# Performance work log

Measured on AMD Instinct MI355X. Metric: run time of the kernel, lower is better.

Reference implementation:

```python
import jax, jax.numpy as jnp
import numpy as np

B, T, C = 4, 2048, 1024
H = 16
D = C // H  # 64


def setup_inputs() -> dict:
    key = jax.random.key(0)
    ks = jax.random.split(key, 3)
    scale = 1.0 / np.sqrt(C)
    return {
        "x": jax.random.normal(ks[0], (B, T, C), dtype=jnp.float32),
        "W_attn": jax.random.normal(ks[1], (C, 3 * C), dtype=jnp.float32) * scale,
        "b_attn": jnp.zeros((3 * C,), dtype=jnp.float32),
        "W_proj": jax.random.normal(ks[2], (C, C), dtype=jnp.float32) * scale,
        "b_proj": jnp.zeros((C,), dtype=jnp.float32),
    }


def reference(x, W_attn, b_attn, W_proj, b_proj):
    b, t, c = x.shape
    qkv = x @ W_attn + b_attn                      # [B,T,3C]
    q, k, v = jnp.split(qkv, 3, axis=-1)           # each [B,T,C]
    to_heads = lambda z: z.reshape(b, t, H, D).transpose(0, 2, 1, 3)  # [B,H,T,D]
    q, k, v = to_heads(q), to_heads(k), to_heads(v)
    scores = jnp.einsum("bhtd,bhsd->bhts", q, k) / jnp.sqrt(jnp.float32(D))
    causal = jnp.tril(jnp.ones((t, t), dtype=bool))  # [T,T]
    scores = jnp.where(causal[None, None], scores, jnp.finfo(scores.dtype).min)
    attn = jax.nn.softmax(scores, axis=-1)           # [B,H,T,T]
    out = jnp.einsum("bhts,bhsd->bhtd", attn, v)     # [B,H,T,D]
    out = out.transpose(0, 2, 1, 3).reshape(b, t, c)
    return out @ W_proj + b_proj
```

## Files before the change

### kernel.cpp

```cpp
#include <hip/hip_runtime.h>
#include <hip/hip_bf16.h>

typedef __bf16 bf16_t;
typedef __attribute__((ext_vector_type(8))) __bf16 bf16x8;
typedef __attribute__((ext_vector_type(4))) float f32x4;
typedef __attribute__((ext_vector_type(4))) unsigned short u16x4;

#define B_DIM 4
#define T_DIM 2048
#define C_DIM 1024
#define H_DIM 16
#define D_DIM 64
#define M_TOK (B_DIM * T_DIM)
#define N_QKV (3 * C_DIM)
#define NT    (T_DIM / 64)
#define KSTR  72
#define CSC   0.18033688011112042f

__device__ __forceinline__ void gload_lds16(const bf16_t* g, bf16_t* l) {
  __builtin_amdgcn_global_load_lds((const __attribute__((address_space(1))) void*)(g),
                                   (__attribute__((address_space(3))) void*)(l), 16, 0, 0);
}

__global__ void cvt_f32_to_bf16(const float* __restrict__ in, bf16_t* __restrict__ out, int n4) {
  int i = blockIdx.x * blockDim.x + threadIdx.x;
  if (i >= n4) return;
  float4 v = ((const float4*)in)[i];
  struct alignas(8) bv4 { bf16_t x, y, z, w; };
  bv4 o;
  o.x = (bf16_t)v.x; o.y = (bf16_t)v.y; o.z = (bf16_t)v.z; o.w = (bf16_t)v.w;
  ((bv4*)out)[i] = o;
}

__global__ void transpose_f32_to_bf16(const float* __restrict__ in, bf16_t* __restrict__ out,
                                      int K, int N) {
  __shared__ float tile[32][33];
  int bx = blockIdx.x * 32;
  int by = blockIdx.y * 32;
  int tx = threadIdx.x, ty = threadIdx.y;
#pragma unroll
  for (int i = 0; i < 32; i += 8)
    tile[ty + i][tx] = in[(size_t)(by + ty + i) * N + bx + tx];
  __syncthreads();
#pragma unroll
  for (int i = 0; i < 32; i += 8)
    out[(size_t)(bx + ty + i) * K + by + tx] = (bf16_t)tile[tx][ty + i];
}

#define BM 128
#define BN 128
#define BK 32

__global__ __launch_bounds__(256, 4)
void gemm_bt_bias(const bf16_t* __restrict__ A, const bf16_t* __restrict__ Bt,
                  const float* __restrict__ bias, bf16_t* __restrict__ Cb,
                  int M, int N, int K) {
  __shared__ alignas(16) bf16_t As[BM * BK];
  __shared__ alignas(16) bf16_t Bs[BN * BK];
  const int tid = threadIdx.x;
  const int lane = tid & 63;
  const int wave = tid >> 6;
  const int wr = (wave >> 1) * 64, wc = (wave & 1) * 64;
  const int quad = lane >> 4, l16 = lane & 15;
  const int row0 = blockIdx.x * BM, col0 = blockIdx.y * BN;

  const int srow = wave * 32 + (lane >> 2);
  const int scol = (lane & 3) * 8;
  const bf16_t* Ag = A + (size_t)(row0 + srow) * K + scol;
  const bf16_t* Bg = Bt + (size_t)(col0 + srow) * K + scol;
  bf16_t* AsW = &As[(wave * 32) * BK];
  bf16_t* BsW = &Bs[(wave * 32) * BK];

  f32x4 acc[4][4];
#pragma unroll
  for (int i = 0; i < 4; ++i)
#pragma unroll
    for (int j = 0; j < 4; ++j)
      acc[i][j] = (f32x4){0.f, 0.f, 0.f, 0.f};

  for (int k0 = 0; k0 < K; k0 += BK) {
    __syncthreads();
    gload_lds16(Ag + k0, AsW);
    gload_lds16(Ag + k0 + (size_t)16 * K, AsW + 16 * BK);
    gload_lds16(Bg + k0, BsW);
    gload_lds16(Bg + k0 + (size_t)16 * K, BsW + 16 * BK);
    __syncthreads();
    bf16x8 af[4], bfr[4];
#pragma unroll
    for (int i = 0; i < 4; ++i)
      af[i] = *(const bf16x8*)&As[(wr + i * 16 + l16) * BK + quad * 8];
#pragma unroll
    for (int j = 0; j < 4; ++j)
      bfr[j] = *(const bf16x8*)&Bs[(wc + j * 16 + l16) * BK + quad * 8];
#pragma unroll
    for (int i = 0; i < 4; ++i)
#pragma unroll
      for (int j = 0; j < 4; ++j)
        acc[i][j] = __builtin_amdgcn_mfma_f32_16x16x32_bf16(af[i], bfr[j], acc[i][j], 0, 0, 0);
  }

#pragma unroll
  for (int i = 0; i < 4; ++i)
#pragma unroll
    for (int j = 0; j < 4; ++j) {
      int col = col0 + wc + j * 16 + l16;
      float bv = bias[col];
#pragma unroll
      for (int r = 0; r < 4; ++r) {
        int row = row0 + wr + i * 16 + quad * 4 + r;
        Cb[(size_t)row * N + col] = (bf16_t)(acc[i][j][r] + bv);
      }
    }
}

__global__ __launch_bounds__(256, 4)
void gemm_bt_bias_n64(const bf16_t* __restrict__ A, const bf16_t* __restrict__ Bt,
                      const float* __restrict__ bias, float* __restrict__ Cf,
                      int M, int N, int K) {
  __shared__ alignas(16) bf16_t As[BM * BK];
  __shared__ alignas(16) bf16_t Bs[64 * BK];
  const int tid = threadIdx.x;
  const int lane = tid & 63;
  const int wave = tid >> 6;
  const int wr = (wave >> 1) * 64, wc = (wave & 1) * 32;
  const int quad = lane >> 4, l16 = lane & 15;
  const int row0 = blockIdx.x * BM, col0 = blockIdx.y * 64;

  const int sr = lane >> 2;
  const int scol = (lane & 3) * 8;
  const bf16_t* Ag = A + (size_t)(row0 + wave * 32 + sr) * K + scol;
  const bf16_t* Bg = Bt + (size_t)(col0 + wave * 16 + sr) * K + scol;
  bf16_t* AsW = &As[(wave * 32) * BK];
  bf16_t* BsW = &Bs[(wave * 16) * BK];

  f32x4 acc[4][2];
#pragma unroll
  for (int i = 0; i < 4; ++i)
#pragma unroll
    for (int j = 0; j < 2; ++j)
      acc[i][j] = (f32x4){0.f, 0.f, 0.f, 0.f};

  for (int k0 = 0; k0 < K; k0 += BK) {
    __syncthreads();
    gload_lds16(Ag + k0, AsW);
    gload_lds16(Ag + k0 + (size_t)16 * K, AsW + 16 * BK);
    gload_lds16(Bg + k0, BsW);
    __syncthreads();
    bf16x8 af[4], bfr[2];
#pragma unroll
    for (int i = 0; i < 4; ++i)
      af[i] = *(const bf16x8*)&As[(wr + i * 16 + l16) * BK + quad * 8];
#pragma unroll
    for (int j = 0; j < 2; ++j)
      bfr[j] = *(const bf16x8*)&Bs[(wc + j * 16 + l16) * BK + quad * 8];
#pragma unroll
    for (int i = 0; i < 4; ++i)
#pragma unroll
      for (int j = 0; j < 2; ++j)
        acc[i][j] = __builtin_amdgcn_mfma_f32_16x16x32_bf16(af[i], bfr[j], acc[i][j], 0, 0, 0);
  }

#pragma unroll
  for (int i = 0; i < 4; ++i)
#pragma unroll
    for (int j = 0; j < 2; ++j) {
      int col = col0 + wc + j * 16 + l16;
      float bv = bias[col];
#pragma unroll
      for (int r = 0; r < 4; ++r) {
        int row = row0 + wr + i * 16 + quad * 4 + r;
        Cf[(size_t)row * N + col] = acc[i][j][r] + bv;
      }
    }
}

__device__ __forceinline__ float exp_row_sum(f32x4 sv[4], bool diag, bf16_t* PsW,
                                             int l16, int quad, int wave) {
  if (diag) {
    const int qr = wave * 16 + l16;
#pragma unroll
    for (int ct = 0; ct < 4; ++ct)
#pragma unroll
      for (int r = 0; r < 4; ++r)
        if (ct * 16 + quad * 4 + r > qr) sv[ct][r] = -INFINITY;
  }
  float rsum = 0.f;
#pragma unroll
  for (int ct = 0; ct < 4; ++ct) {
    u16x4 pk;
#pragma unroll
    for (int r = 0; r < 4; ++r) {
      float p = __builtin_amdgcn_exp2f(sv[ct][r] * CSC);
      rsum += p;
      pk[r] = __builtin_bit_cast(unsigned short, (bf16_t)p);
    }
    *(u16x4*)&PsW[l16 * KSTR + ct * 16 + quad * 4] = pk;
  }
  rsum += __shfl_xor(rsum, 16);
  rsum += __shfl_xor(rsum, 32);
  return rsum;
}

__global__ __launch_bounds__(256, 4)
void attn_fwd(const bf16_t* __restrict__ qkv, bf16_t* __restrict__ out) {
  __shared__ alignas(16) bf16_t Ks[64 * KSTR];
  __shared__ alignas(16) bf16_t Vt[64 * KSTR];
  __shared__ alignas(16) bf16_t Ps[4 * 16 * KSTR];

  const int tid = threadIdx.x;
  const int lane = tid & 63;
  const int wave = tid >> 6;
  const int quad = lane >> 4, l16 = lane & 15;
  const int qlo = blockIdx.x;
  const int qhi = NT - 1 - qlo;
  const int h = blockIdx.y, b = blockIdx.z;
  const size_t tokBase = (size_t)b * T_DIM;

  const bf16_t* qpl = qkv + (tokBase + qlo * 64 + wave * 16 + l16) * N_QKV + h * D_DIM;
  const bf16_t* qph = qkv + (tokBase + qhi * 64 + wave * 16 + l16) * N_QKV + h * D_DIM;
  bf16x8 ql0 = *(const bf16x8*)(qpl + quad * 8);
  bf16x8 ql1 = *(const bf16x8*)(qpl + 32 + quad * 8);
  bf16x8 qh0 = *(const bf16x8*)(qph + quad * 8);
  bf16x8 qh1 = *(const bf16x8*)(qph + 32 + quad * 8);

  f32x4 ol[4], oh[4];
#pragma unroll
  for (int dt = 0; dt < 4; ++dt) {
    ol[dt] = (f32x4){0.f, 0.f, 0.f, 0.f};
    oh[dt] = (f32x4){0.f, 0.f, 0.f, 0.f};
  }
  float ll = 0.f, lh = 0.f;

  const int tx = tid & 15, ty = tid >> 4;
  const int vswz = ((tx >> 2) & 3) * 8;
  bf16_t* PsW = &Ps[wave * 16 * KSTR];
  const f32x4 zero4 = (f32x4){0.f, 0.f, 0.f, 0.f};

  u16x4 kreg[4], vreg[4];
  const bf16_t* kb0 = qkv + (tokBase + ty * 4) * N_QKV + h * D_DIM + C_DIM + tx * 4;
#pragma unroll
  for (int r = 0; r < 4; ++r) kreg[r] = *(const u16x4*)(kb0 + (size_t)r * N_QKV);
#pragma unroll
  for (int r = 0; r < 4; ++r) vreg[r] = *(const u16x4*)(kb0 + (size_t)r * N_QKV + C_DIM);

  for (int t = 0; t <= qhi; ++t) {
    const bool lo = (t <= qlo);
    __syncthreads();
#pragma unroll
    for (int r = 0; r < 4; ++r)
      *(u16x4*)&Ks[(ty * 4 + r) * KSTR + tx * 4] = kreg[r];
#pragma unroll
    for (int i = 0; i < 4; ++i) {
      u16x4 p = (u16x4){vreg[0][i], vreg[1][i], vreg[2][i], vreg[3][i]};
      *(u16x4*)&Vt[(tx * 4 + i) * KSTR + ((ty * 4) ^ vswz)] = p;
    }
    __syncthreads();
    if (t < qhi) {
      const bf16_t* kb = qkv + (tokBase + (t + 1) * 64 + ty * 4) * N_QKV + h * D_DIM + C_DIM + tx * 4;
#pragma unroll
      for (int r = 0; r < 4; ++r) kreg[r] = *(const u16x4*)(kb + (size_t)r * N_QKV);
#pragma unroll
      for (int r = 0; r < 4; ++r) vreg[r] = *(const u16x4*)(kb + (size_t)r * N_QKV + C_DIM);
    }

    f32x4 svl[4], svh[4];
#pragma unroll
    for (int ct = 0; ct < 4; ++ct) {
      bf16x8 kf0 = *(const bf16x8*)&Ks[(ct * 16 + l16) * KSTR + quad * 8];
      bf16x8 kf1 = *(const bf16x8*)&Ks[(ct * 16 + l16) * KSTR + 32 + quad * 8];
      if (lo) {
        svl[ct] = __builtin_amdgcn_mfma_f32_16x16x32_bf16(kf0, ql0, zero4, 0, 0, 0);
        svl[ct] = __builtin_amdgcn_mfma_f32_16x16x32_bf16(kf1, ql1, svl[ct], 0, 0, 0);
      }
      svh[ct] = __builtin_amdgcn_mfma_f32_16x16x32_bf16(kf0, qh0, zero4, 0, 0, 0);
      svh[ct] = __builtin_amdgcn_mfma_f32_16x16x32_bf16(kf1, qh1, svh[ct], 0, 0, 0);
    }

    bf16x8 pl0, pl1, ph0, ph1;
    if (lo) {
      ll += exp_row_sum(svl, t == qlo, PsW, l16, quad, wave);
      pl0 = *(const bf16x8*)&PsW[l16 * KSTR + quad * 8];
      pl1 = *(const bf16x8*)&PsW[l16 * KSTR + 32 + quad * 8];
    }
    lh += exp_row_sum(svh, t == qhi, PsW, l16, quad, wave);
    ph0 = *(const bf16x8*)&PsW[l16 * KSTR + quad * 8];
    ph1 = *(const bf16x8*)&PsW[l16 * KSTR + 32 + quad * 8];

#pragma unroll
    for (int dt = 0; dt < 4; ++dt) {
      const int vcol = (quad * 8) ^ ((dt & 3) * 8);
      bf16x8 vf0 = *(const bf16x8*)&Vt[(dt * 16 + l16) * KSTR + vcol];
      bf16x8 vf1 = *(const bf16x8*)&Vt[(dt * 16 + l16) * KSTR + 32 + vcol];
      if (lo) {
        ol[dt] = __builtin_amdgcn_mfma_f32_16x16x32_bf16(vf0, pl0, ol[dt], 0, 0, 0);
        ol[dt] = __builtin_amdgcn_mfma_f32_16x16x32_bf16(vf1, pl1, ol[dt], 0, 0, 0);
      }
      oh[dt] = __builtin_amdgcn_mfma_f32_16x16x32_bf16(vf0, ph0, oh[dt], 0, 0, 0);
      oh[dt] = __builtin_amdgcn_mfma_f32_16x16x32_bf16(vf1, ph1, oh[dt], 0, 0, 0);
    }
  }

  struct alignas(8) bh4 { bf16_t a, b, c, d; };
  {
    float rl = 1.0f / ll;
    bf16_t* op = out + (tokBase + qlo * 64 + wave * 16 + l16) * C_DIM + h * D_DIM;
#pragma unroll
    for (int dt = 0; dt < 4; ++dt) {
      bh4 v = {(bf16_t)(ol[dt][0] * rl), (bf16_t)(ol[dt][1] * rl),
               (bf16_t)(ol[dt][2] * rl), (bf16_t)(ol[dt][3] * rl)};
      *(bh4*)(op + dt * 16 + quad * 4) = v;
    }
  }
  {
    float rl = 1.0f / lh;
    bf16_t* op = out + (tokBase + qhi * 64 + wave * 16 + l16) * C_DIM + h * D_DIM;
#pragma unroll
    for (int dt = 0; dt < 4; ++dt) {
      bh4 v = {(bf16_t)(oh[dt][0] * rl), (bf16_t)(oh[dt][1] * rl),
               (bf16_t)(oh[dt][2] * rl), (bf16_t)(oh[dt][3] * rl)};
      *(bh4*)(op + dt * 16 + quad * 4) = v;
    }
  }
}

extern "C" void kernel_launch(void* const* d_in, const int* in_sizes, int n_in,
                              void* d_out, int out_size, void* d_ws, size_t ws_size,
                              hipStream_t stream) {
  const float* x      = (const float*)d_in[0];
  const float* W_attn = (const float*)d_in[1];
  const float* b_attn = (const float*)d_in[2];
  const float* W_proj = (const float*)d_in[3];
  const float* b_proj = (const float*)d_in[4];
  float* out = (float*)d_out;

  char* ws = (char*)d_ws;
  bf16_t* xb   = (bf16_t*)ws;  ws += (size_t)M_TOK * C_DIM * 2;
  bf16_t* Wat  = (bf16_t*)ws;  ws += (size_t)N_QKV * C_DIM * 2;
  bf16_t* Wpt  = (bf16_t*)ws;  ws += (size_t)C_DIM * C_DIM * 2;
  bf16_t* qkv  = (bf16_t*)ws;  ws += (size_t)M_TOK * N_QKV * 2;
  bf16_t* attn = (bf16_t*)ws;  ws += (size_t)M_TOK * C_DIM * 2;

  {
    int n4 = (M_TOK * C_DIM) / 4;
    cvt_f32_to_bf16<<<n4 / 256, 256, 0, stream>>>(x, xb, n4);
  }
  transpose_f32_to_bf16<<<dim3(N_QKV / 32, C_DIM / 32), dim3(32, 8), 0, stream>>>(W_attn, Wat, C_DIM, N_QKV);
  transpose_f32_to_bf16<<<dim3(C_DIM / 32, C_DIM / 32), dim3(32, 8), 0, stream>>>(W_proj, Wpt, C_DIM, C_DIM);

  gemm_bt_bias<<<dim3(M_TOK / BM, N_QKV / BN), 256, 0, stream>>>(
      xb, Wat, b_attn, qkv, M_TOK, N_QKV, C_DIM);

  attn_fwd<<<dim3(NT / 2, H_DIM, B_DIM), 256, 0, stream>>>(qkv, attn);

  gemm_bt_bias_n64<<<dim3(M_TOK / BM, C_DIM / 64), 256, 0, stream>>>(
      attn, Wpt, b_proj, out, M_TOK, C_DIM, C_DIM);
}
```

Baseline: 266.2 us.

## Keep softmax probabilities in registers and use one query tile per block

The attention kernel no longer pairs a low and high query tile per block. Each block now handles a single tile, with a rotated blockIdx-to-tile mapping to spread causal work across the grid. The P tile no longer round-trips through LDS: the V transpose store uses a permuted column layout so the exponentiated scores can be packed directly into the MFMA B operand. This removes the Ps buffer and its LDS traffic, and the launch bound is raised to 8 blocks, but per-block work becomes uneven and K/V tiles are reloaded once per query tile.

```diff
diff --git a/kernel.cpp b/kernel.cpp
--- a/kernel.cpp
+++ b/kernel.cpp
@@ -5,6 +5,7 @@
 typedef __attribute__((ext_vector_type(8))) __bf16 bf16x8;
 typedef __attribute__((ext_vector_type(4))) float f32x4;
 typedef __attribute__((ext_vector_type(4))) unsigned short u16x4;
+typedef __attribute__((ext_vector_type(4))) unsigned int u32x4;
 
 #define B_DIM 4
 #define T_DIM 2048
@@ -174,66 +175,31 @@
     }
 }
 
-__device__ __forceinline__ float exp_row_sum(f32x4 sv[4], bool diag, bf16_t* PsW,
-                                             int l16, int quad, int wave) {
-  if (diag) {
-    const int qr = wave * 16 + l16;
-#pragma unroll
-    for (int ct = 0; ct < 4; ++ct)
-#pragma unroll
-      for (int r = 0; r < 4; ++r)
-        if (ct * 16 + quad * 4 + r > qr) sv[ct][r] = -INFINITY;
-  }
-  float rsum = 0.f;
-#pragma unroll
-  for (int ct = 0; ct < 4; ++ct) {
-    u16x4 pk;
-#pragma unroll
-    for (int r = 0; r < 4; ++r) {
-      float p = __builtin_amdgcn_exp2f(sv[ct][r] * CSC);
-      rsum += p;
-      pk[r] = __builtin_bit_cast(unsigned short, (bf16_t)p);
-    }
-    *(u16x4*)&PsW[l16 * KSTR + ct * 16 + quad * 4] = pk;
-  }
-  rsum += __shfl_xor(rsum, 16);
-  rsum += __shfl_xor(rsum, 32);
-  return rsum;
-}
-
-__global__ __launch_bounds__(256, 4)
+__global__ __launch_bounds__(256, 8)
 void attn_fwd(const bf16_t* __restrict__ qkv, bf16_t* __restrict__ out) {
   __shared__ alignas(16) bf16_t Ks[64 * KSTR];
   __shared__ alignas(16) bf16_t Vt[64 * KSTR];
-  __shared__ alignas(16) bf16_t Ps[4 * 16 * KSTR];
 
   const int tid = threadIdx.x;
   const int lane = tid & 63;
   const int wave = tid >> 6;
   const int quad = lane >> 4, l16 = lane & 15;
-  const int qlo = blockIdx.x;
-  const int qhi = NT - 1 - qlo;
   const int h = blockIdx.y, b = blockIdx.z;
+  const int q = (int)((blockIdx.x + h + 2 * b) & 31);
   const size_t tokBase = (size_t)b * T_DIM;
 
-  const bf16_t* qpl = qkv + (tokBase + qlo * 64 + wave * 16 + l16) * N_QKV + h * D_DIM;
-  const bf16_t* qph = qkv + (tokBase + qhi * 64 + wave * 16 + l16) * N_QKV + h * D_DIM;
-  bf16x8 ql0 = *(const bf16x8*)(qpl + quad * 8);
-  bf16x8 ql1 = *(const bf16x8*)(qpl + 32 + quad * 8);
-  bf16x8 qh0 = *(const bf16x8*)(qph + quad * 8);
-  bf16x8 qh1 = *(const bf16x8*)(qph + 32 + quad * 8);
-
-  f32x4 ol[4], oh[4];
-#pragma unroll
-  for (int dt = 0; dt < 4; ++dt) {
-    ol[dt] = (f32x4){0.f, 0.f, 0.f, 0.f};
-    oh[dt] = (f32x4){0.f, 0.f, 0.f, 0.f};
-  }
-  float ll = 0.f, lh = 0.f;
+  const bf16_t* qp = qkv + (tokBase + q * 64 + wave * 16 + l16) * N_QKV + h * D_DIM;
+  bf16x8 q0 = *(const bf16x8*)(qp + quad * 8);
+  bf16x8 q1 = *(const bf16x8*)(qp + 32 + quad * 8);
+
+  f32x4 o[4];
+#pragma unroll
+  for (int dt = 0; dt < 4; ++dt) o[dt] = (f32x4){0.f, 0.f, 0.f, 0.f};
+  float lsum = 0.f;
 
   const int tx = tid & 15, ty = tid >> 4;
   const int vswz = ((tx >> 2) & 3) * 8;
-  bf16_t* PsW = &Ps[wave * 16 * KSTR];
+  const int vcol = (8 * (ty & 3) + 4 * ((ty >> 2) & 1) + 32 * (ty >> 3)) ^ vswz;
   const f32x4 zero4 = (f32x4){0.f, 0.f, 0.f, 0.f};
 
   u16x4 kreg[4], vreg[4];
@@ -243,8 +209,7 @@
 #pragma unroll
   for (int r = 0; r < 4; ++r) vreg[r] = *(const u16x4*)(kb0 + (size_t)r * N_QKV + C_DIM);
 
-  for (int t = 0; t <= qhi; ++t) {
-    const bool lo = (t <= qlo);
+  for (int t = 0; t <= q; ++t) {
     __syncthreads();
 #pragma unroll
     for (int r = 0; r < 4; ++r)
@@ -252,10 +217,10 @@
 #pragma unroll
     for (int i = 0; i < 4; ++i) {
       u16x4 p = (u16x4){vreg[0][i], vreg[1][i], vreg[2][i], vreg[3][i]};
-      *(u16x4*)&Vt[(tx * 4 + i) * KSTR + ((ty * 4) ^ vswz)] = p;
-    }
-    __syncthreads();
-    if (t < qhi) {
+      *(u16x4*)&Vt[(tx * 4 + i) * KSTR + vcol] = p;
+    }
+    __syncthreads();
+    if (t < q) {
       const bf16_t* kb = qkv + (tokBase + (t + 1) * 64 + ty * 4) * N_QKV + h * D_DIM + C_DIM + tx * 4;
 #pragma unroll
       for (int r = 0; r < 4; ++r) kreg[r] = *(const u16x4*)(kb + (size_t)r * N_QKV);
@@ -263,61 +228,65 @@
       for (int r = 0; r < 4; ++r) vreg[r] = *(const u16x4*)(kb + (size_t)r * N_QKV + C_DIM);
     }
 
-    f32x4 svl[4], svh[4];
+    f32x4 sv[4];
 #pragma unroll
     for (int ct = 0; ct < 4; ++ct) {
       bf16x8 kf0 = *(const bf16x8*)&Ks[(ct * 16 + l16) * KSTR + quad * 8];
       bf16x8 kf1 = *(const bf16x8*)&Ks[(ct * 16 + l16) * KSTR + 32 + quad * 8];
-      if (lo) {
-        svl[ct] = __builtin_amdgcn_mfma_f32_16x16x32_bf16(kf0, ql0, zero4, 0, 0, 0);
-        svl[ct] = __builtin_amdgcn_mfma_f32_16x16x32_bf16(kf1, ql1, svl[ct], 0, 0, 0);
-      }
-      svh[ct] = __builtin_amdgcn_mfma_f32_16x16x32_bf16(kf0, qh0, zero4, 0, 0, 0);
-      svh[ct] = __builtin_amdgcn_mfma_f32_16x16x32_bf16(kf1, qh1, svh[ct], 0, 0, 0);
-    }
-
-    bf16x8 pl0, pl1, ph0, ph1;
-    if (lo) {
-      ll += exp_row_sum(svl, t == qlo, PsW, l16, quad, wave);
-      pl0 = *(const bf16x8*)&PsW[l16 * KSTR + quad * 8];
-      pl1 = *(const bf16x8*)&PsW[l16 * KSTR + 32 + quad * 8];
-    }
-    lh += exp_row_sum(svh, t == qhi, PsW, l16, quad, wave);
-    ph0 = *(const bf16x8*)&PsW[l16 * KSTR + quad * 8];
-    ph1 = *(const bf16x8*)&PsW[l16 * KSTR + 32 + quad * 8];
+      sv[ct] = __builtin_amdgcn_mfma_f32_16x16x32_bf16(kf0, q0, zero4, 0, 0, 0);
+      sv[ct] = __builtin_amdgcn_mfma_f32_16x16x32_bf16(kf1, q1, sv[ct], 0, 0, 0);
+    }
+    if (t == q) {
+      const int qr = wave * 16 + l16;
+#pragma unroll
+      for (int ct = 0; ct < 4; ++ct)
+#pragma unroll
+        for (int r = 0; r < 4; ++r)
+          if (ct * 16 + quad * 4 + r > qr) sv[ct][r] = -INFINITY;
+    }
+
+    float rsum = 0.f;
+    unsigned int lw[8];
+    struct alignas(4) bpair { bf16_t lo, hi; };
+#pragma unroll
+    for (int ct = 0; ct < 4; ++ct) {
+      float e0 = __builtin_amdgcn_exp2f(sv[ct][0] * CSC);
+      float e1 = __builtin_amdgcn_exp2f(sv[ct][1] * CSC);
+      float e2 = __builtin_amdgcn_exp2f(sv[ct][2] * CSC);
+      float e3 = __builtin_amdgcn_exp2f(sv[ct][3] * CSC);
+      rsum += (e0 + e1) + (e2 + e3);
+      bpair w0 = {(bf16_t)e0, (bf16_t)e1};
+      bpair w1 = {(bf16_t)e2, (bf16_t)e3};
+      lw[ct * 2 + 0] = __builtin_bit_cast(unsigned int, w0);
+      lw[ct * 2 + 1] = __builtin_bit_cast(unsigned int, w1);
+    }
+    rsum += __shfl_xor(rsum, 16);
+    rsum += __shfl_xor(rsum, 32);
+    lsum += rsum;
+
+    u32x4 pw0 = (u32x4){lw[0], lw[1], lw[2], lw[3]};
+    u32x4 pw1 = (u32x4){lw[4], lw[5], lw[6], lw[7]};
+    bf16x8 p0 = __builtin_bit_cast(bf16x8, pw0);
+    bf16x8 p1 = __builtin_bit_cast(bf16x8, pw1);
 
 #pragma unroll
     for (int dt = 0; dt < 4; ++dt) {
-      const int vcol = (quad * 8) ^ ((dt & 3) * 8);
-      bf16x8 vf0 = *(const bf16x8*)&Vt[(dt * 16 + l16) * KSTR + vcol];
-      bf16x8 vf1 = *(const bf16x8*)&Vt[(dt * 16 + l16) * KSTR + 32 + vcol];
-      if (lo) {
-        ol[dt] = __builtin_amdgcn_mfma_f32_16x16x32_bf16(vf0, pl0, ol[dt], 0, 0, 0);
-        ol[dt] = __builtin_amdgcn_mfma_f32_16x16x32_bf16(vf1, pl1, ol[dt], 0, 0, 0);
-      }
-      oh[dt] = __builtin_amdgcn_mfma_f32_16x16x32_bf16(vf0, ph0, oh[dt], 0, 0, 0);
-      oh[dt] = __builtin_amdgcn_mfma_f32_16x16x32_bf16(vf1, ph1, oh[dt], 0, 0, 0);
+      const int vc = (quad * 8) ^ (dt * 8);
+      bf16x8 vf0 = *(const bf16x8*)&Vt[(dt * 16 + l16) * KSTR + vc];
+      bf16x8 vf1 = *(const bf16x8*)&Vt[(dt * 16 + l16) * KSTR + 32 + vc];
+      o[dt] = __builtin_amdgcn_mfma_f32_16x16x32_bf16(vf0, p0, o[dt], 0, 0, 0);
+      o[dt] = __builtin_amdgcn_mfma_f32_16x16x32_bf16(vf1, p1, o[dt], 0, 0, 0);
     }
   }
 
   struct alignas(8) bh4 { bf16_t a, b, c, d; };
   {
-    float rl = 1.0f / ll;
-    bf16_t* op = out + (tokBase + qlo * 64 + wave * 16 + l16) * C_DIM + h * D_DIM;
+    float rl = 1.0f / lsum;
+    bf16_t* op = out + (tokBase + q * 64 + wave * 16 + l16) * C_DIM + h * D_DIM;
 #pragma unroll
     for (int dt = 0; dt < 4; ++dt) {
-      bh4 v = {(bf16_t)(ol[dt][0] * rl), (bf16_t)(ol[dt][1] * rl),
-               (bf16_t)(ol[dt][2] * rl), (bf16_t)(ol[dt][3] * rl)};
-      *(bh4*)(op + dt * 16 + quad * 4) = v;
-    }
-  }
-  {
-    float rl = 1.0f / lh;
-    bf16_t* op = out + (tokBase + qhi * 64 + wave * 16 + l16) * C_DIM + h * D_DIM;
-#pragma unroll
-    for (int dt = 0; dt < 4; ++dt) {
-      bh4 v = {(bf16_t)(oh[dt][0] * rl), (bf16_t)(oh[dt][1] * rl),
-               (bf16_t)(oh[dt][2] * rl), (bf16_t)(oh[dt][3] * rl)};
+      bh4 v = {(bf16_t)(o[dt][0] * rl), (bf16_t)(o[dt][1] * rl),
+               (bf16_t)(o[dt][2] * rl), (bf16_t)(o[dt][3] * rl)};
       *(bh4*)(op + dt * 16 + quad * 4) = v;
     }
   }
@@ -350,7 +319,7 @@
   gemm_bt_bias<<<dim3(M_TOK / BM, N_QKV / BN), 256, 0, stream>>>(
       xb, Wat, b_attn, qkv, M_TOK, N_QKV, C_DIM);
 
-  attn_fwd<<<dim3(NT / 2, H_DIM, B_DIM), 256, 0, stream>>>(qkv, attn);
+  attn_fwd<<<dim3(NT, H_DIM, B_DIM), 256, 0, stream>>>(qkv, attn);
 
   gemm_bt_bias_n64<<<dim3(M_TOK / BM, C_DIM / 64), 256, 0, stream>>>(
       attn, Wpt, b_proj, out, M_TOK, C_DIM, C_DIM);
```

Measured after the change: 317.9 us. 1.19x slower.

## Keep softmax probabilities in registers by permuting V's key layout in LDS

Applied to the files above, without the earlier changes.

Drops the per-wave LDS staging buffer for P. The exponentiated scores are now packed straight into the MFMA B-operand registers, and the V tile is stored in LDS with its key dimension permuted so it matches the register layout of P from the S MFMA output. This removes an LDS write/read round trip and the LDS footprint of P on every key tile. The cost is a more intricate index mapping for V, and correctness depends on that permutation matching exactly.

```diff
diff --git a/kernel.cpp b/kernel.cpp
--- a/kernel.cpp
+++ b/kernel.cpp
@@ -5,6 +5,7 @@
 typedef __attribute__((ext_vector_type(8))) __bf16 bf16x8;
 typedef __attribute__((ext_vector_type(4))) float f32x4;
 typedef __attribute__((ext_vector_type(4))) unsigned short u16x4;
+typedef __attribute__((ext_vector_type(4))) unsigned int u32x4;
 
 #define B_DIM 4
 #define T_DIM 2048
@@ -174,38 +175,10 @@
     }
 }
 
-__device__ __forceinline__ float exp_row_sum(f32x4 sv[4], bool diag, bf16_t* PsW,
-                                             int l16, int quad, int wave) {
-  if (diag) {
-    const int qr = wave * 16 + l16;
-#pragma unroll
-    for (int ct = 0; ct < 4; ++ct)
-#pragma unroll
-      for (int r = 0; r < 4; ++r)
-        if (ct * 16 + quad * 4 + r > qr) sv[ct][r] = -INFINITY;
-  }
-  float rsum = 0.f;
-#pragma unroll
-  for (int ct = 0; ct < 4; ++ct) {
-    u16x4 pk;
-#pragma unroll
-    for (int r = 0; r < 4; ++r) {
-      float p = __builtin_amdgcn_exp2f(sv[ct][r] * CSC);
-      rsum += p;
-      pk[r] = __builtin_bit_cast(unsigned short, (bf16_t)p);
-    }
-    *(u16x4*)&PsW[l16 * KSTR + ct * 16 + quad * 4] = pk;
-  }
-  rsum += __shfl_xor(rsum, 16);
-  rsum += __shfl_xor(rsum, 32);
-  return rsum;
-}
-
 __global__ __launch_bounds__(256, 4)
 void attn_fwd(const bf16_t* __restrict__ qkv, bf16_t* __restrict__ out) {
   __shared__ alignas(16) bf16_t Ks[64 * KSTR];
   __shared__ alignas(16) bf16_t Vt[64 * KSTR];
-  __shared__ alignas(16) bf16_t Ps[4 * 16 * KSTR];
 
   const int tid = threadIdx.x;
   const int lane = tid & 63;
@@ -233,7 +206,7 @@
 
   const int tx = tid & 15, ty = tid >> 4;
   const int vswz = ((tx >> 2) & 3) * 8;
-  bf16_t* PsW = &Ps[wave * 16 * KSTR];
+  const int vcol = (8 * (ty & 3) + 4 * ((ty >> 2) & 1) + 32 * (ty >> 3)) ^ vswz;
   const f32x4 zero4 = (f32x4){0.f, 0.f, 0.f, 0.f};
 
   u16x4 kreg[4], vreg[4];
@@ -252,7 +225,7 @@
 #pragma unroll
     for (int i = 0; i < 4; ++i) {
       u16x4 p = (u16x4){vreg[0][i], vreg[1][i], vreg[2][i], vreg[3][i]};
-      *(u16x4*)&Vt[(tx * 4 + i) * KSTR + ((ty * 4) ^ vswz)] = p;
+      *(u16x4*)&Vt[(tx * 4 + i) * KSTR + vcol] = p;
     }
     __syncthreads();
     if (t < qhi) {
@@ -275,22 +248,77 @@
       svh[ct] = __builtin_amdgcn_mfma_f32_16x16x32_bf16(kf0, qh0, zero4, 0, 0, 0);
       svh[ct] = __builtin_amdgcn_mfma_f32_16x16x32_bf16(kf1, qh1, svh[ct], 0, 0, 0);
     }
-
+    if (t == qlo) {
+      const int qr = wave * 16 + l16;
+#pragma unroll
+      for (int ct = 0; ct < 4; ++ct)
+#pragma unroll
+        for (int r = 0; r < 4; ++r)
+          if (ct * 16 + quad * 4 + r > qr) svl[ct][r] = -INFINITY;
+    }
+    if (t == qhi) {
+      const int qr = wave * 16 + l16;
+#pragma unroll
+      for (int ct = 0; ct < 4; ++ct)
+#pragma unroll
+        for (int r = 0; r < 4; ++r)
+          if (ct * 16 + quad * 4 + r > qr) svh[ct][r] = -INFINITY;
+    }
+
+    struct alignas(4) bpair { bf16_t lo, hi; };
     bf16x8 pl0, pl1, ph0, ph1;
     if (lo) {
-      ll += exp_row_sum(svl, t == qlo, PsW, l16, quad, wave);
-      pl0 = *(const bf16x8*)&PsW[l16 * KSTR + quad * 8];
-      pl1 = *(const bf16x8*)&PsW[l16 * KSTR + 32 + quad * 8];
-    }
-    lh += exp_row_sum(svh, t == qhi, PsW, l16, quad, wave);
-    ph0 = *(const bf16x8*)&PsW[l16 * KSTR + quad * 8];
-    ph1 = *(const bf16x8*)&PsW[l16 * KSTR + 32 + quad * 8];
+      float rsum = 0.f;
+      unsigned int lw[8];
+#pragma unroll
+      for (int ct = 0; ct < 4; ++ct) {
+        float e0 = __builtin_amdgcn_exp2f(svl[ct][0] * CSC);
+        float e1 = __builtin_amdgcn_exp2f(svl[ct][1] * CSC);
+        float e2 = __builtin_amdgcn_exp2f(svl[ct][2] * CSC);
+        float e3 = __builtin_amdgcn_exp2f(svl[ct][3] * CSC);
+        rsum += (e0 + e1) + (e2 + e3);
+        bpair w0 = {(bf16_t)e0, (bf16_t)e1};
+        bpair w1 = {(bf16_t)e2, (bf16_t)e3};
+        lw[ct * 2 + 0] = __builtin_bit_cast(unsigned int, w0);
+        lw[ct * 2 + 1] = __builtin_bit_cast(unsigned int, w1);
+      }
+      rsum += __shfl_xor(rsum, 16);
+      rsum += __shfl_xor(rsum, 32);
+      ll += rsum;
+      u32x4 pw0 = (u32x4){lw[0], lw[1], lw[2], lw[3]};
+      u32x4 pw1 = (u32x4){lw[4], lw[5], lw[6], lw[7]};
+      pl0 = __builtin_bit_cast(bf16x8, pw0);
+      pl1 = __builtin_bit_cast(bf16x8, pw1);
+    }
+    {
+      float rsum = 0.f;
+      unsigned int lw[8];
+#pragma unroll
+      for (int ct = 0; ct < 4; ++ct) {
+        float e0 = __builtin_amdgcn_exp2f(svh[ct][0] * CSC);
+        float e1 = __builtin_amdgcn_exp2f(svh[ct][1] * CSC);
+        float e2 = __builtin_amdgcn_exp2f(svh[ct][2] * CSC);
+        float e3 = __builtin_amdgcn_exp2f(svh[ct][3] * CSC);
+        rsum += (e0 + e1) + (e2 + e3);
+        bpair w0 = {(bf16_t)e0, (bf16_t)e1};
+        bpair w1 = {(bf16_t)e2, (bf16_t)e3};
+        lw[ct * 2 + 0] = __builtin_bit_cast(unsigned int, w0);
+        lw[ct * 2 + 1] = __builtin_bit_cast(unsigned int, w1);
+      }
+      rsum += __shfl_xor(rsum, 16);
+      rsum += __shfl_xor(rsum, 32);
+      lh += rsum;
+      u32x4 pw0 = (u32x4){lw[0], lw[1], lw[2], lw[3]};
+      u32x4 pw1 = (u32x4){lw[4], lw[5], lw[6], lw[7]};
+      ph0 = __builtin_bit_cast(bf16x8, pw0);
+      ph1 = __builtin_bit_cast(bf16x8, pw1);
+    }
 
 #pragma unroll
     for (int dt = 0; dt < 4; ++dt) {
-      const int vcol = (quad * 8) ^ ((dt & 3) * 8);
-      bf16x8 vf0 = *(const bf16x8*)&Vt[(dt * 16 + l16) * KSTR + vcol];
-      bf16x8 vf1 = *(const bf16x8*)&Vt[(dt * 16 + l16) * KSTR + 32 + vcol];
+      const int vc = (quad * 8) ^ (dt * 8);
+      bf16x8 vf0 = *(const bf16x8*)&Vt[(dt * 16 + l16) * KSTR + vc];
+      bf16x8 vf1 = *(const bf16x8*)&Vt[(dt * 16 + l16) * KSTR + 32 + vc];
       if (lo) {
         ol[dt] = __builtin_amdgcn_mfma_f32_16x16x32_bf16(vf0, pl0, ol[dt], 0, 0, 0);
         ol[dt] = __builtin_amdgcn_mfma_f32_16x16x32_bf16(vf1, pl1, ol[dt], 0, 0, 0);
```

New measurement: 273.7 us. 1.03x slower.
